# Optimization experiments

Measured on AMD Instinct MI355X. Metric: run time of the kernel, lower is better.

Reference implementation:

```python
import jax, jax.numpy as jnp
import numpy as np

N_NODES = 50000
N_EDGES = 800000
N_GRAPHS = 256


def setup_inputs() -> dict:
    key = jax.random.key(0)
    ks = jax.random.split(key, 20)
    s = 0.05
    return {
        "x": jax.random.normal(ks[0], (N_NODES, 128), jnp.float32),
        "edge_index": jax.random.randint(ks[1], (2, N_EDGES), 0, N_NODES, jnp.int64),
        "batch_index": jnp.sort(jax.random.randint(ks[2], (N_NODES,), 0, N_GRAPHS, jnp.int64)),
        "mol_features": jax.random.normal(ks[3], (N_GRAPHS, 256), jnp.float32),
        "gcn_W": jax.random.normal(ks[4], (3, 128, 128), jnp.float32) * s,
        "gcn_b": jax.random.normal(ks[5], (3, 128), jnp.float32) * s,
        "gcn_out_W": jax.random.normal(ks[6], (128, 128), jnp.float32) * s,
        "gcn_out_b": jax.random.normal(ks[7], (128,), jnp.float32) * s,
        "mlp_W": jax.random.normal(ks[8], (2, 256, 256), jnp.float32) * s,
        "mlp_b": jax.random.normal(ks[9], (2, 256), jnp.float32) * s,
        "mlp_out_W": jax.random.normal(ks[10], (64, 256), jnp.float32) * s,
        "mlp_out_b": jax.random.normal(ks[11], (64,), jnp.float32) * s,
        "pred_W1": jax.random.normal(ks[12], (256, 192), jnp.float32) * s,
        "pred_b1": jax.random.normal(ks[13], (256,), jnp.float32) * s,
        "pred_W2": jax.random.normal(ks[14], (256, 256), jnp.float32) * s,
        "pred_b2": jax.random.normal(ks[15], (256,), jnp.float32) * s,
        "out_W": jax.random.normal(ks[16], (1, 256), jnp.float32) * s,
        "out_b": jax.random.normal(ks[17], (1,), jnp.float32) * s,
    }


def reference(x, edge_index, batch_index, mol_features,
              gcn_W, gcn_b, gcn_out_W, gcn_out_b,
              mlp_W, mlp_b, mlp_out_W, mlp_out_b,
              pred_W1, pred_b1, pred_W2, pred_b2, out_W, out_b):
    N = x.shape[0]
    E = edge_index.shape[1]
    G = mol_features.shape[0]
    row, col = edge_index[0], edge_index[1]

    # GCN normalization with self-loops (PyG gcn_norm, symmetric):
    # deg[i] = in-degree(i) + 1 (self loop); norm_e = d^-1/2[row] * d^-1/2[col]
    deg = jax.ops.segment_sum(jnp.ones((E,), x.dtype), col, num_segments=N) + 1.0
    dinv = jax.lax.rsqrt(deg)
    enorm = (dinv[row] * dinv[col])[:, None]     # [E,1]
    self_c = (dinv * dinv)[:, None]              # [N,1] self-loop coefficient

    h1 = x
    for i in range(gcn_W.shape[0]):
        h = h1 @ gcn_W[i].T                      # per-node transform [N,128]
        agg = jax.ops.segment_sum(h[row] * enorm, col, num_segments=N)
        h1 = jax.nn.relu(agg + self_c * h + gcn_b[i])
    h1 = h1 @ gcn_out_W.T + gcn_out_b            # final GCN-branch Linear (no relu)

    # global_mean_pool over batch_index -> [G,128]
    sums = jax.ops.segment_sum(h1, batch_index, num_segments=G)
    counts = jax.ops.segment_sum(jnp.ones((N,), x.dtype), batch_index, num_segments=G)
    h1 = sums / jnp.maximum(counts, 1.0)[:, None]

    # MLP branch: relu after every linear (including last)
    h2 = mol_features
    for i in range(mlp_W.shape[0]):
        h2 = jax.nn.relu(h2 @ mlp_W[i].T + mlp_b[i])
    h2 = jax.nn.relu(h2 @ mlp_out_W.T + mlp_out_b)

    h = jnp.concatenate([h1, h2], axis=1)        # [G,192]
    h = jax.nn.relu(h @ pred_W1.T + pred_b1)
    h = jax.nn.relu(h @ pred_W2.T + pred_b2)
    return h @ out_W.T + out_b                   # [G,1]
```

## Files before the change

### kernel.cpp

```cpp
#include <hip/hip_runtime.h>


typedef __attribute__((ext_vector_type(8))) short short8;
typedef __attribute__((ext_vector_type(4))) float f32x4;

__device__ __forceinline__ unsigned short f2bf(float f) {
    union { float f; unsigned u; } c; c.f = f;
    unsigned u = c.u;
    unsigned r = u + 0x7FFFu + ((u >> 16) & 1u);
    return (unsigned short)(r >> 16);
}
__device__ __forceinline__ float bflo(unsigned w) {
    union { unsigned u; float f; } c; c.u = w << 16; return c.f;
}
__device__ __forceinline__ float bfhi(unsigned w) {
    union { unsigned u; float f; } c; c.u = w & 0xFFFF0000u; return c.f;
}

__global__ void k_zero(int* deg, float* pool, float* cnt, int* csr_pad,
                       int N, int G) {
    int i = blockIdx.x * blockDim.x + threadIdx.x;
    if (i < N) deg[i] = 0;
    if (i < G * 128) pool[i] = 0.f;
    if (i < G) cnt[i] = 0.f;
    if (i < 32) csr_pad[i] = 0;
}

__global__ void k_castx(const float* __restrict__ x, unsigned short* __restrict__ xb,
                        int total8) {
    int i = blockIdx.x * blockDim.x + threadIdx.x;
    if (i >= total8) return;
    const float4* s = (const float4*)(x + (size_t)i * 8);
    float4 a = s[0], b = s[1];
    uint4 o;
    o.x = ((unsigned)f2bf(a.y) << 16) | f2bf(a.x);
    o.y = ((unsigned)f2bf(a.w) << 16) | f2bf(a.z);
    o.z = ((unsigned)f2bf(b.y) << 16) | f2bf(b.x);
    o.w = ((unsigned)f2bf(b.w) << 16) | f2bf(b.z);
    *(uint4*)(xb + (size_t)i * 8) = o;
}

__global__ void k_wcast(const float* __restrict__ gcnW, uint4* __restrict__ Wb) {
    int cid = blockIdx.x * 256 + threadIdx.x;
    if (cid >= 3 * 2048) return;
    int l = cid >> 11, rem = cid & 2047;
    int o = rem >> 4, c = rem & 15;
    const float4* s = (const float4*)(gcnW + (size_t)l * 16384 + o * 128 + c * 8);
    float4 a = s[0], b = s[1];
    uint4 v;
    v.x = ((unsigned)f2bf(a.y) << 16) | f2bf(a.x);
    v.y = ((unsigned)f2bf(a.w) << 16) | f2bf(a.z);
    v.z = ((unsigned)f2bf(b.y) << 16) | f2bf(b.x);
    v.w = ((unsigned)f2bf(b.w) << 16) | f2bf(b.z);
    Wb[(l << 11) | (o << 4) | (c ^ (o & 15))] = v;
}

__global__ void k_degree(const int* __restrict__ col, int* __restrict__ deg, int E) {
    int e = blockIdx.x * blockDim.x + threadIdx.x;
    if (e < E) atomicAdd(&deg[col[e]], 1);
}

__global__ __launch_bounds__(256) void k_scan1(const int* __restrict__ deg,
                                               int* __restrict__ bsum, int N) {
    int t = threadIdx.x;
    int i = blockIdx.x * 256 + t;
    int v = (i < N) ? deg[i] : 0;
    #pragma unroll
    for (int off = 32; off > 0; off >>= 1) v += __shfl_xor(v, off, 64);
    __shared__ int ws[4];
    if ((t & 63) == 0) ws[t >> 6] = v;
    __syncthreads();
    if (t == 0) bsum[blockIdx.x] = ws[0] + ws[1] + ws[2] + ws[3];
}

__global__ __launch_bounds__(256) void k_scan2(int* __restrict__ bsum, int NB) {
    int t = threadIdx.x, lane = t & 63, wv = t >> 6;
    int v = (t < NB) ? bsum[t] : 0;
    int x = v;
    #pragma unroll
    for (int off = 1; off < 64; off <<= 1) {
        int u = __shfl_up(x, off, 64);
        if (lane >= off) x += u;
    }
    __shared__ int ws[4];
    if (lane == 63) ws[wv] = x;
    __syncthreads();
    int woff = 0;
    for (int w = 0; w < wv; ++w) woff += ws[w];
    if (t < NB) bsum[t] = woff + x - v;
}

__global__ __launch_bounds__(256) void k_scan3(const int* __restrict__ deg,
                                               const int* __restrict__ bsum,
                                               int* __restrict__ rowptr,
                                               int* __restrict__ cursor,
                                               float* __restrict__ dinv,
                                               int N, int E) {
    int t = threadIdx.x, lane = t & 63, wv = t >> 6;
    int i = blockIdx.x * 256 + t;
    int v = (i < N) ? deg[i] : 0;
    int x = v;
    #pragma unroll
    for (int off = 1; off < 64; off <<= 1) {
        int u = __shfl_up(x, off, 64);
        if (lane >= off) x += u;
    }
    __shared__ int ws[4];
    if (lane == 63) ws[wv] = x;
    __syncthreads();
    int woff = 0;
    for (int w = 0; w < wv; ++w) woff += ws[w];
    int excl = bsum[blockIdx.x] + woff + (x - v);
    if (i < N) {
        rowptr[i] = excl;
        cursor[i] = excl;
        dinv[i] = rsqrtf((float)v + 1.0f);
    }
    if (i == 0) rowptr[N] = E;
}

__global__ void k_scatter(const int* __restrict__ row, const int* __restrict__ col,
                          const float* __restrict__ dinv,
                          int* __restrict__ cursor,
                          unsigned long long* __restrict__ csr, int E) {
    int e = blockIdx.x * blockDim.x + threadIdx.x;
    if (e < E) {
        int pos = atomicAdd(&cursor[col[e]], 1);
        int r = row[e];
        union { float f; unsigned u; } w; w.f = dinv[r];
        csr[pos] = ((unsigned long long)(unsigned)r << 32) | w.u;
    }
}

__global__ __launch_bounds__(256) void k_agg(const unsigned short* __restrict__ h,
                                             unsigned short* __restrict__ y,
                                             const float* __restrict__ dinv,
                                             const int* __restrict__ rowptr,
                                             const uint2* __restrict__ csr,
                                             int N) {
    const int lane = threadIdx.x & 63;
    const int n = blockIdx.x * 4 + (threadIdx.x >> 6);
    if (n >= N) return;
    const int fg = lane & 15;
    const int slot = lane >> 4;
    const int s = rowptr[n], e = rowptr[n + 1];

    float acc[8] = {0.f, 0.f, 0.f, 0.f, 0.f, 0.f, 0.f, 0.f};
    for (int base = s; base < e; base += 16) {
        int li = base + fg;
        uint2 pk = csr[li];
        float w_l = (li < e) ? bflo(pk.x >> 16) : 0.f;
        w_l = (li < e) ? __uint_as_float(pk.x) : 0.f;
        int src_l = (int)pk.y;
        #pragma unroll
        for (int i = 0; i < 4; ++i) {
            int j = i * 4 + slot;
            int src = __shfl(src_l, j, 16);
            float w = __shfl(w_l, j, 16);
            uint4 v = *(const uint4*)(h + (size_t)src * 128 + fg * 8);
            acc[0] += w * bflo(v.x); acc[1] += w * bfhi(v.x);
            acc[2] += w * bflo(v.y); acc[3] += w * bfhi(v.y);
            acc[4] += w * bflo(v.z); acc[5] += w * bfhi(v.z);
            acc[6] += w * bflo(v.w); acc[7] += w * bfhi(v.w);
        }
    }
    #pragma unroll
    for (int r = 0; r < 8; ++r) {
        acc[r] += __shfl_xor(acc[r], 16, 64);
        acc[r] += __shfl_xor(acc[r], 32, 64);
    }
    if (slot == 0) {
        float dn = dinv[n], dn2 = dn * dn;
        uint4 hv = *(const uint4*)(h + (size_t)n * 128 + fg * 8);
        float sv[8] = {bflo(hv.x), bfhi(hv.x), bflo(hv.y), bfhi(hv.y),
                       bflo(hv.z), bfhi(hv.z), bflo(hv.w), bfhi(hv.w)};
        unsigned short ob[8];
        #pragma unroll
        for (int r = 0; r < 8; ++r) ob[r] = f2bf(acc[r] * dn + dn2 * sv[r]);
        uint4 o;
        o.x = ((unsigned)ob[1] << 16) | ob[0];
        o.y = ((unsigned)ob[3] << 16) | ob[2];
        o.z = ((unsigned)ob[5] << 16) | ob[4];
        o.w = ((unsigned)ob[7] << 16) | ob[6];
        *(uint4*)(y + (size_t)n * 128 + fg * 8) = o;
    }
}

__global__ __launch_bounds__(256) void k_mm(const unsigned short* __restrict__ A,
                                            const uint4* __restrict__ Wb,
                                            const float* __restrict__ bias,
                                            unsigned short* __restrict__ C, int N) {
    __shared__ uint4 Wsh[2048];
    const int tid = threadIdx.x;
    #pragma unroll
    for (int it = 0; it < 8; ++it)
        Wsh[tid + it * 256] = Wb[tid + it * 256];

    const int lane = tid & 63;
    const int wv = tid >> 6;
    const int l15 = lane & 15, quad = lane >> 4;
    const int arow_i = blockIdx.x * 64 + wv * 16 + l15;
    const unsigned short* arow = A + (size_t)min(arow_i, N - 1) * 128;

    f32x4 acc[8];
    #pragma unroll
    for (int ct = 0; ct < 8; ++ct) acc[ct] = (f32x4){0.f, 0.f, 0.f, 0.f};

    __syncthreads();
    #pragma unroll
    for (int kiter = 0; kiter < 4; ++kiter) {
        short8 af = *(const short8*)(arow + kiter * 32 + quad * 8);
        const int cswz = (kiter * 4 + quad) ^ l15;
        #pragma unroll
        for (int ct = 0; ct < 8; ++ct) {
            short8 bf = *(const short8*)(&Wsh[((ct * 16 + l15) << 4) | cswz]);
            acc[ct] = __builtin_amdgcn_mfma_f32_16x16x32_bf16(af, bf, acc[ct], 0, 0, 0);
        }
    }

    const int rbase = blockIdx.x * 64 + wv * 16 + quad * 4;
    #pragma unroll
    for (int ct = 0; ct < 8; ++ct) {
        int colc = ct * 16 + l15;
        float bcol = bias[colc];
        #pragma unroll
        for (int r = 0; r < 4; ++r) {
            int rr = rbase + r;
            if (rr < N) {
                float v = fmaxf(acc[ct][r] + bcol, 0.f);
                C[(size_t)rr * 128 + colc] = f2bf(v);
            }
        }
    }
}

__global__ __launch_bounds__(256) void k_pool(const unsigned short* __restrict__ h,
                                              const int* __restrict__ batch,
                                              float* __restrict__ pool,
                                              float* __restrict__ cnt, int N) {
    int t = threadIdx.x;
    int fg = t & 15, sg = t >> 4;
    int n0 = blockIdx.x * 512 + sg * 32;
    if (n0 >= N) return;
    int n1 = min(n0 + 32, N);
    int gprev = batch[n0];
    float racc[8] = {0.f, 0.f, 0.f, 0.f, 0.f, 0.f, 0.f, 0.f};
    float rcnt = 0.f;
    for (int n = n0; n < n1; ++n) {
        int g = batch[n];
        if (g != gprev) {
            float* dst = pool + (size_t)gprev * 128 + fg * 8;
            #pragma unroll
            for (int r = 0; r < 8; ++r) atomicAdd(dst + r, racc[r]);
            if (fg == 0) atomicAdd(&cnt[gprev], rcnt);
            #pragma unroll
            for (int r = 0; r < 8; ++r) racc[r] = 0.f;
            rcnt = 0.f; gprev = g;
        }
        uint4 v = *(const uint4*)(h + (size_t)n * 128 + fg * 8);
        racc[0] += bflo(v.x); racc[1] += bfhi(v.x);
        racc[2] += bflo(v.y); racc[3] += bfhi(v.y);
        racc[4] += bflo(v.z); racc[5] += bfhi(v.z);
        racc[6] += bflo(v.w); racc[7] += bfhi(v.w);
        rcnt += 1.f;
    }
    float* dst = pool + (size_t)gprev * 128 + fg * 8;
    #pragma unroll
    for (int r = 0; r < 8; ++r) atomicAdd(dst + r, racc[r]);
    if (fg == 0) atomicAdd(&cnt[gprev], rcnt);
}

__global__ __launch_bounds__(256) void k_head(
    const float* __restrict__ pool, const float* __restrict__ cnt,
    const float* __restrict__ gcnoW, const float* __restrict__ gcnob,
    const float* __restrict__ mol,
    const float* __restrict__ mlpW, const float* __restrict__ mlpb,
    const float* __restrict__ mloW, const float* __restrict__ mlob,
    const float* __restrict__ pW1, const float* __restrict__ pb1,
    const float* __restrict__ pW2, const float* __restrict__ pb2,
    const float* __restrict__ oW, const float* __restrict__ ob,
    float* __restrict__ out) {
    int g = blockIdx.x, t = threadIdx.x;
    __shared__ float s0[256], s1[256], s2[192], mean[128], red[256];

    s0[t] = mol[(size_t)g * 256 + t];
    if (t < 128) {
        float c = cnt[g];
        mean[t] = pool[(size_t)g * 128 + t] / fmaxf(c, 1.f);
    }
    __syncthreads();

    float acc = mlpb[t];
    {
        const float4* w = (const float4*)(mlpW + (size_t)t * 256);
        #pragma unroll 4
        for (int k4 = 0; k4 < 64; ++k4) {
            float4 wv = w[k4];
            acc += s0[k4*4+0]*wv.x + s0[k4*4+1]*wv.y + s0[k4*4+2]*wv.z + s0[k4*4+3]*wv.w;
        }
    }
    s1[t] = fmaxf(acc, 0.f);
    __syncthreads();

    acc = mlpb[256 + t];
    {
        const float4* w = (const float4*)(mlpW + 65536 + (size_t)t * 256);
        #pragma unroll 4
        for (int k4 = 0; k4 < 64; ++k4) {
            float4 wv = w[k4];
            acc += s1[k4*4+0]*wv.x + s1[k4*4+1]*wv.y + s1[k4*4+2]*wv.z + s1[k4*4+3]*wv.w;
        }
    }
    s0[t] = fmaxf(acc, 0.f);
    __syncthreads();

    if (t < 64) {
        float a2 = mlob[t];
        const float4* w = (const float4*)(mloW + (size_t)t * 256);
        #pragma unroll 4
        for (int k4 = 0; k4 < 64; ++k4) {
            float4 wv = w[k4];
            a2 += s0[k4*4+0]*wv.x + s0[k4*4+1]*wv.y + s0[k4*4+2]*wv.z + s0[k4*4+3]*wv.w;
        }
        s2[128 + t] = fmaxf(a2, 0.f);
    } else if (t < 192) {
        int o = t - 64;
        float a2 = gcnob[o];
        const float4* w = (const float4*)(gcnoW + (size_t)o * 128);
        #pragma unroll 4
        for (int k4 = 0; k4 < 32; ++k4) {
            float4 wv = w[k4];
            a2 += mean[k4*4+0]*wv.x + mean[k4*4+1]*wv.y + mean[k4*4+2]*wv.z + mean[k4*4+3]*wv.w;
        }
        s2[o] = a2;
    }
    __syncthreads();

    acc = pb1[t];
    {
        const float4* w = (const float4*)(pW1 + (size_t)t * 192);
        #pragma unroll 4
        for (int k4 = 0; k4 < 48; ++k4) {
            float4 wv = w[k4];
            acc += s2[k4*4+0]*wv.x + s2[k4*4+1]*wv.y + s2[k4*4+2]*wv.z + s2[k4*4+3]*wv.w;
        }
    }
    s1[t] = fmaxf(acc, 0.f);
    __syncthreads();

    acc = pb2[t];
    {
        const float4* w = (const float4*)(pW2 + (size_t)t * 256);
        #pragma unroll 4
        for (int k4 = 0; k4 < 64; ++k4) {
            float4 wv = w[k4];
            acc += s1[k4*4+0]*wv.x + s1[k4*4+1]*wv.y + s1[k4*4+2]*wv.z + s1[k4*4+3]*wv.w;
        }
    }
    s0[t] = fmaxf(acc, 0.f);
    __syncthreads();

    red[t] = s0[t] * oW[t];
    __syncthreads();
    for (int off = 128; off > 0; off >>= 1) {
        if (t < off) red[t] += red[t + off];
        __syncthreads();
    }
    if (t == 0) out[g] = red[0] + ob[0];
}

extern "C" void kernel_launch(void* const* d_in, const int* in_sizes, int n_in,
                              void* d_out, int out_size, void* d_ws, size_t ws_size,
                              hipStream_t stream) {
    const float* x     = (const float*)d_in[0];
    const int*   ei    = (const int*)d_in[1];
    const int*   batch = (const int*)d_in[2];
    const float* mol   = (const float*)d_in[3];
    const float* gcnW  = (const float*)d_in[4];
    const float* gcnb  = (const float*)d_in[5];
    const float* gcnoW = (const float*)d_in[6];
    const float* gcnob = (const float*)d_in[7];
    const float* mlpW  = (const float*)d_in[8];
    const float* mlpb  = (const float*)d_in[9];
    const float* mloW  = (const float*)d_in[10];
    const float* mlob  = (const float*)d_in[11];
    const float* pW1   = (const float*)d_in[12];
    const float* pb1   = (const float*)d_in[13];
    const float* pW2   = (const float*)d_in[14];
    const float* pb2   = (const float*)d_in[15];
    const float* oW    = (const float*)d_in[16];
    const float* ob    = (const float*)d_in[17];

    const int N = in_sizes[0] / 128;
    const int E = in_sizes[1] / 2;
    const int G = in_sizes[3] / 256;
    const int* row = ei;
    const int* col = ei + E;

    char* p = (char*)d_ws;
    auto alloc = [&](size_t bytes) {
        char* q = p;
        p += (bytes + 255) & ~(size_t)255;
        return (void*)q;
    };
    int*    deg    = (int*)alloc((size_t)N * 4);
    int*    rowptr = (int*)alloc((size_t)(N + 1) * 4);
    int*    cursor = (int*)alloc((size_t)N * 4);
    unsigned long long* csr = (unsigned long long*)alloc((size_t)(E + 16) * 8);
    float*  dinv   = (float*)alloc((size_t)N * 4);
    unsigned short* xb   = (unsigned short*)alloc((size_t)N * 128 * 2);
    unsigned short* bufA = (unsigned short*)alloc((size_t)N * 128 * 2);
    unsigned short* bufB = (unsigned short*)alloc((size_t)N * 128 * 2);
    uint4*  Wb     = (uint4*)alloc((size_t)3 * 2048 * 16);
    float*  pool   = (float*)alloc((size_t)G * 128 * 4);
    float*  cnt    = (float*)alloc((size_t)G * 4);
    int*    bsum   = (int*)alloc(256 * 4);

    const int NB = (N + 255) / 256;

    k_zero<<<NB, 256, 0, stream>>>(deg, pool, cnt, (int*)(csr + E), N, G);
    k_castx<<<(N * 16 + 255) / 256, 256, 0, stream>>>(x, xb, N * 16);
    k_wcast<<<24, 256, 0, stream>>>(gcnW, Wb);
    k_degree<<<(E + 255) / 256, 256, 0, stream>>>(col, deg, E);
    k_scan1<<<NB, 256, 0, stream>>>(deg, bsum, N);
    k_scan2<<<1, 256, 0, stream>>>(bsum, NB);
    k_scan3<<<NB, 256, 0, stream>>>(deg, bsum, rowptr, cursor, dinv, N, E);
    k_scatter<<<(E + 255) / 256, 256, 0, stream>>>(row, col, dinv, cursor, csr, E);

    const int mmblocks = (N + 63) / 64;
    const int aggblocks = (N + 3) / 4;
    const unsigned short* src = xb;
    for (int l = 0; l < 3; ++l) {
        k_agg<<<aggblocks, 256, 0, stream>>>(src, bufA, dinv, rowptr,
                                             (const uint2*)csr, N);
        k_mm<<<mmblocks, 256, 0, stream>>>(bufA, Wb + (size_t)l * 2048,
                                           gcnb + (size_t)l * 128, bufB, N);
        src = bufB;
    }
    k_pool<<<(N + 511) / 512, 256, 0, stream>>>(bufB, batch, pool, cnt, N);
    k_head<<<G, 256, 0, stream>>>(pool, cnt, gcnoW, gcnob, mol, mlpW, mlpb,
                                  mloW, mlob, pW1, pb1, pW2, pb2, oW, ob,
                                  (float*)d_out);
}
```

Measured before the change: 394.1 us.

## Build CSR via bucketed counting sort, use 16-bit indices, fold dinv into features

Replaces the per-node atomic degree/scan/scatter CSR build with a bucketed two-level counting sort. Edges are histogrammed and binned per 64-node bucket, then sorted locally in shared memory. Neighbour lists shrink to 16-bit source indices with no per-edge weight. The symmetric normalisation is folded into the features instead: x is pre-scaled by dinv, each GEMM epilogue multiplies by dinv, and aggregation scales by dinv[n] once. This cuts edge-list bandwidth and per-edge multiplies. In exchange it assumes N < 65536 and that the bucket count fits a fixed 784-entry shared histogram, and it adds a single-block scan.

```diff
diff --git a/kernel.cpp b/kernel.cpp
--- a/kernel.cpp
+++ b/kernel.cpp
@@ -3,6 +3,10 @@
 
 typedef __attribute__((ext_vector_type(8))) short short8;
 typedef __attribute__((ext_vector_type(4))) float f32x4;
+
+#define BKT 64
+#define SL 8
+#define NBINBLK 256
 
 __device__ __forceinline__ unsigned short f2bf(float f) {
     union { float f; unsigned u; } c; c.f = f;
@@ -17,26 +21,128 @@
     union { unsigned u; float f; } c; c.u = w & 0xFFFF0000u; return c.f;
 }
 
-__global__ void k_zero(int* deg, float* pool, float* cnt, int* csr_pad,
-                       int N, int G) {
+__global__ void k_zero(int* ghist, float* pool, float* cnt, int* csr_pad,
+                       int M, int N, int G) {
     int i = blockIdx.x * blockDim.x + threadIdx.x;
-    if (i < N) deg[i] = 0;
+    if (i < M) ghist[i] = 0;
     if (i < G * 128) pool[i] = 0.f;
     if (i < G) cnt[i] = 0.f;
-    if (i < 32) csr_pad[i] = 0;
-}
-
-__global__ void k_castx(const float* __restrict__ x, unsigned short* __restrict__ xb,
-                        int total8) {
+    if (i < 8) csr_pad[i] = 0;
+}
+
+__global__ __launch_bounds__(256) void k_hist(const int* __restrict__ col,
+                                              int* __restrict__ ghist,
+                                              int E, int C, int NBK) {
+    __shared__ int h[784];
+    int t = threadIdx.x;
+    for (int i = t; i < NBK; i += 256) h[i] = 0;
+    __syncthreads();
+    const int x = blockIdx.x & (SL - 1);
+    int e0 = blockIdx.x * C, e1 = min(E, e0 + C);
+    for (int e = e0 + t; e < e1; e += 256) atomicAdd(&h[col[e] >> 6], 1);
+    __syncthreads();
+    for (int b = t; b < NBK; b += 256) {
+        int c = h[b];
+        if (c) atomicAdd(&ghist[b * SL + x], c);
+    }
+}
+
+__global__ __launch_bounds__(256) void k_bscan(const int* __restrict__ ghist,
+                                               int* __restrict__ gbase,
+                                               int* __restrict__ cur,
+                                               int* __restrict__ rowptr,
+                                               int M, int N, int E) {
+    __shared__ int ws[4];
+    __shared__ int s_carry;
+    int t = threadIdx.x, lane = t & 63, wv = t >> 6;
+    if (t == 0) s_carry = 0;
+    __syncthreads();
+    for (int base = 0; base < M; base += 256) {
+        int i = base + t;
+        int v = (i < M) ? ghist[i] : 0;
+        int x = v;
+        #pragma unroll
+        for (int off = 1; off < 64; off <<= 1) {
+            int u = __shfl_up(x, off, 64);
+            if (lane >= off) x += u;
+        }
+        if (lane == 63) ws[wv] = x;
+        __syncthreads();
+        int woff = 0;
+        for (int w = 0; w < wv; ++w) woff += ws[w];
+        int excl = s_carry + woff + (x - v);
+        if (i < M) { gbase[i] = excl; cur[i] = excl; }
+        __syncthreads();
+        if (t == 255) s_carry = excl + v;
+        __syncthreads();
+    }
+    if (t == 0) { gbase[M] = E; rowptr[N] = E; }
+}
+
+__global__ __launch_bounds__(256) void k_bin(const int* __restrict__ row,
+                                             const int* __restrict__ col,
+                                             int* __restrict__ cur,
+                                             unsigned* __restrict__ gbin,
+                                             int E, int C) {
+    const int x = blockIdx.x & (SL - 1);
+    int e0 = blockIdx.x * C, e1 = min(E, e0 + C);
+    for (int e = e0 + threadIdx.x; e < e1; e += 256) {
+        int c = col[e];
+        int si = (c >> 6) * SL + x;
+        int pos = atomicAdd(&cur[si], 1);
+        gbin[pos] = (unsigned)row[e] | ((unsigned)(c & 63) << 16);
+    }
+}
+
+__global__ __launch_bounds__(256) void k_csr(const unsigned* __restrict__ gbin,
+                                             const int* __restrict__ gbase,
+                                             int* __restrict__ rowptr,
+                                             float* __restrict__ dinv,
+                                             unsigned short* __restrict__ csrf,
+                                             int N) {
+    const int b = blockIdx.x, t = threadIdx.x;
+    __shared__ int cnt[64], lcur[64];
+    if (t < 64) cnt[t] = 0;
+    __syncthreads();
+    const int beg = gbase[b * SL], end = gbase[(b + 1) * SL];
+    for (int i = beg + t; i < end; i += 256)
+        atomicAdd(&cnt[gbin[i] >> 16], 1);
+    __syncthreads();
+    if (t < 64) {
+        int v = cnt[t], x = v;
+        #pragma unroll
+        for (int off = 1; off < 64; off <<= 1) {
+            int u = __shfl_up(x, off, 64);
+            if (t >= off) x += u;
+        }
+        int excl = x - v;
+        lcur[t] = excl;
+        int node = b * 64 + t;
+        if (node < N) {
+            rowptr[node] = beg + excl;
+            dinv[node] = rsqrtf((float)v + 1.0f);
+        }
+    }
+    __syncthreads();
+    for (int i = beg + t; i < end; i += 256) {
+        unsigned v = gbin[i];
+        int p = atomicAdd(&lcur[v >> 16], 1);
+        csrf[beg + p] = (unsigned short)(v & 0xFFFFu);
+    }
+}
+
+__global__ void k_castx(const float* __restrict__ x, const float* __restrict__ dinv,
+                        unsigned short* __restrict__ xb, int total8) {
     int i = blockIdx.x * blockDim.x + threadIdx.x;
     if (i >= total8) return;
+    float d = dinv[i >> 4];
     const float4* s = (const float4*)(x + (size_t)i * 8);
     float4 a = s[0], b = s[1];
     uint4 o;
-    o.x = ((unsigned)f2bf(a.y) << 16) | f2bf(a.x);
-    o.y = ((unsigned)f2bf(a.w) << 16) | f2bf(a.z);
-    o.z = ((unsigned)f2bf(b.y) << 16) | f2bf(b.x);
-    o.w = ((unsigned)f2bf(b.w) << 16) | f2bf(b.z);
+    o.x = ((unsigned)f2bf(d * a.y) << 16) | f2bf(d * a.x);
+    o.y = ((unsigned)f2bf(d * a.w) << 16) | f2bf(d * a.z);
+    o.z = ((unsigned)f2bf(d * b.y) << 16) | f2bf(d * b.x);
+    o.w = ((unsigned)f2bf(d * b.w) << 16) | f2bf(d * b.z);
     *(uint4*)(xb + (size_t)i * 8) = o;
 }
 
@@ -55,88 +161,11 @@
     Wb[(l << 11) | (o << 4) | (c ^ (o & 15))] = v;
 }
 
-__global__ void k_degree(const int* __restrict__ col, int* __restrict__ deg, int E) {
-    int e = blockIdx.x * blockDim.x + threadIdx.x;
-    if (e < E) atomicAdd(&deg[col[e]], 1);
-}
-
-__global__ __launch_bounds__(256) void k_scan1(const int* __restrict__ deg,
-                                               int* __restrict__ bsum, int N) {
-    int t = threadIdx.x;
-    int i = blockIdx.x * 256 + t;
-    int v = (i < N) ? deg[i] : 0;
-    #pragma unroll
-    for (int off = 32; off > 0; off >>= 1) v += __shfl_xor(v, off, 64);
-    __shared__ int ws[4];
-    if ((t & 63) == 0) ws[t >> 6] = v;
-    __syncthreads();
-    if (t == 0) bsum[blockIdx.x] = ws[0] + ws[1] + ws[2] + ws[3];
-}
-
-__global__ __launch_bounds__(256) void k_scan2(int* __restrict__ bsum, int NB) {
-    int t = threadIdx.x, lane = t & 63, wv = t >> 6;
-    int v = (t < NB) ? bsum[t] : 0;
-    int x = v;
-    #pragma unroll
-    for (int off = 1; off < 64; off <<= 1) {
-        int u = __shfl_up(x, off, 64);
-        if (lane >= off) x += u;
-    }
-    __shared__ int ws[4];
-    if (lane == 63) ws[wv] = x;
-    __syncthreads();
-    int woff = 0;
-    for (int w = 0; w < wv; ++w) woff += ws[w];
-    if (t < NB) bsum[t] = woff + x - v;
-}
-
-__global__ __launch_bounds__(256) void k_scan3(const int* __restrict__ deg,
-                                               const int* __restrict__ bsum,
-                                               int* __restrict__ rowptr,
-                                               int* __restrict__ cursor,
-                                               float* __restrict__ dinv,
-                                               int N, int E) {
-    int t = threadIdx.x, lane = t & 63, wv = t >> 6;
-    int i = blockIdx.x * 256 + t;
-    int v = (i < N) ? deg[i] : 0;
-    int x = v;
-    #pragma unroll
-    for (int off = 1; off < 64; off <<= 1) {
-        int u = __shfl_up(x, off, 64);
-        if (lane >= off) x += u;
-    }
-    __shared__ int ws[4];
-    if (lane == 63) ws[wv] = x;
-    __syncthreads();
-    int woff = 0;
-    for (int w = 0; w < wv; ++w) woff += ws[w];
-    int excl = bsum[blockIdx.x] + woff + (x - v);
-    if (i < N) {
-        rowptr[i] = excl;
-        cursor[i] = excl;
-        dinv[i] = rsqrtf((float)v + 1.0f);
-    }
-    if (i == 0) rowptr[N] = E;
-}
-
-__global__ void k_scatter(const int* __restrict__ row, const int* __restrict__ col,
-                          const float* __restrict__ dinv,
-                          int* __restrict__ cursor,
-                          unsigned long long* __restrict__ csr, int E) {
-    int e = blockIdx.x * blockDim.x + threadIdx.x;
-    if (e < E) {
-        int pos = atomicAdd(&cursor[col[e]], 1);
-        int r = row[e];
-        union { float f; unsigned u; } w; w.f = dinv[r];
-        csr[pos] = ((unsigned long long)(unsigned)r << 32) | w.u;
-    }
-}
-
 __global__ __launch_bounds__(256) void k_agg(const unsigned short* __restrict__ h,
                                              unsigned short* __restrict__ y,
                                              const float* __restrict__ dinv,
                                              const int* __restrict__ rowptr,
-                                             const uint2* __restrict__ csr,
+                                             const unsigned short* __restrict__ csrf,
                                              int N) {
     const int lane = threadIdx.x & 63;
     const int n = blockIdx.x * 4 + (threadIdx.x >> 6);
@@ -147,21 +176,19 @@
 
     float acc[8] = {0.f, 0.f, 0.f, 0.f, 0.f, 0.f, 0.f, 0.f};
     for (int base = s; base < e; base += 16) {
-        int li = base + fg;
-        uint2 pk = csr[li];
-        float w_l = (li < e) ? bflo(pk.x >> 16) : 0.f;
-        w_l = (li < e) ? __uint_as_float(pk.x) : 0.f;
-        int src_l = (int)pk.y;
+        int src_l = csrf[base + fg];
         #pragma unroll
         for (int i = 0; i < 4; ++i) {
             int j = i * 4 + slot;
             int src = __shfl(src_l, j, 16);
-            float w = __shfl(w_l, j, 16);
             uint4 v = *(const uint4*)(h + (size_t)src * 128 + fg * 8);
-            acc[0] += w * bflo(v.x); acc[1] += w * bfhi(v.x);
-            acc[2] += w * bflo(v.y); acc[3] += w * bfhi(v.y);
-            acc[4] += w * bflo(v.z); acc[5] += w * bfhi(v.z);
-            acc[6] += w * bflo(v.w); acc[7] += w * bfhi(v.w);
+            bool ok = (base + j) < e;
+            v.x = ok ? v.x : 0u; v.y = ok ? v.y : 0u;
+            v.z = ok ? v.z : 0u; v.w = ok ? v.w : 0u;
+            acc[0] += bflo(v.x); acc[1] += bfhi(v.x);
+            acc[2] += bflo(v.y); acc[3] += bfhi(v.y);
+            acc[4] += bflo(v.z); acc[5] += bfhi(v.z);
+            acc[6] += bflo(v.w); acc[7] += bfhi(v.w);
         }
     }
     #pragma unroll
@@ -170,13 +197,13 @@
         acc[r] += __shfl_xor(acc[r], 32, 64);
     }
     if (slot == 0) {
-        float dn = dinv[n], dn2 = dn * dn;
+        float dn = dinv[n];
         uint4 hv = *(const uint4*)(h + (size_t)n * 128 + fg * 8);
         float sv[8] = {bflo(hv.x), bfhi(hv.x), bflo(hv.y), bfhi(hv.y),
                        bflo(hv.z), bfhi(hv.z), bflo(hv.w), bfhi(hv.w)};
         unsigned short ob[8];
         #pragma unroll
-        for (int r = 0; r < 8; ++r) ob[r] = f2bf(acc[r] * dn + dn2 * sv[r]);
+        for (int r = 0; r < 8; ++r) ob[r] = f2bf(dn * (acc[r] + sv[r]));
         uint4 o;
         o.x = ((unsigned)ob[1] << 16) | ob[0];
         o.y = ((unsigned)ob[3] << 16) | ob[2];
@@ -189,6 +216,7 @@
 __global__ __launch_bounds__(256) void k_mm(const unsigned short* __restrict__ A,
                                             const uint4* __restrict__ Wb,
                                             const float* __restrict__ bias,
+                                            const float* __restrict__ dscale,
                                             unsigned short* __restrict__ C, int N) {
     __shared__ uint4 Wsh[2048];
     const int tid = threadIdx.x;
@@ -219,6 +247,12 @@
     }
 
     const int rbase = blockIdx.x * 64 + wv * 16 + quad * 4;
+    float ds[4];
+    #pragma unroll
+    for (int r = 0; r < 4; ++r) {
+        int rr = rbase + r;
+        ds[r] = (dscale && rr < N) ? dscale[rr] : 1.f;
+    }
     #pragma unroll
     for (int ct = 0; ct < 8; ++ct) {
         int colc = ct * 16 + l15;
@@ -227,7 +261,7 @@
         for (int r = 0; r < 4; ++r) {
             int rr = rbase + r;
             if (rr < N) {
-                float v = fmaxf(acc[ct][r] + bcol, 0.f);
+                float v = fmaxf(acc[ct][r] + bcol, 0.f) * ds[r];
                 C[(size_t)rr * 128 + colc] = f2bf(v);
             }
         }
@@ -397,44 +431,49 @@
     const int* row = ei;
     const int* col = ei + E;
 
+    const int NBK = (N + BKT - 1) / BKT;
+    const int M = NBK * SL;
+    const int C = (E + NBINBLK - 1) / NBINBLK;
+
     char* p = (char*)d_ws;
     auto alloc = [&](size_t bytes) {
         char* q = p;
         p += (bytes + 255) & ~(size_t)255;
         return (void*)q;
     };
-    int*    deg    = (int*)alloc((size_t)N * 4);
     int*    rowptr = (int*)alloc((size_t)(N + 1) * 4);
-    int*    cursor = (int*)alloc((size_t)N * 4);
-    unsigned long long* csr = (unsigned long long*)alloc((size_t)(E + 16) * 8);
     float*  dinv   = (float*)alloc((size_t)N * 4);
+    int*    ghist  = (int*)alloc((size_t)M * 4);
+    int*    gbase  = (int*)alloc((size_t)(M + 1) * 4);
+    int*    cur    = (int*)alloc((size_t)M * 4);
+    unsigned* gbin = (unsigned*)alloc((size_t)E * 4);
+    unsigned short* csrf = (unsigned short*)alloc((size_t)(E + 16) * 2);
     unsigned short* xb   = (unsigned short*)alloc((size_t)N * 128 * 2);
     unsigned short* bufA = (unsigned short*)alloc((size_t)N * 128 * 2);
     unsigned short* bufB = (unsigned short*)alloc((size_t)N * 128 * 2);
     uint4*  Wb     = (uint4*)alloc((size_t)3 * 2048 * 16);
     float*  pool   = (float*)alloc((size_t)G * 128 * 4);
     float*  cnt    = (float*)alloc((size_t)G * 4);
-    int*    bsum   = (int*)alloc(256 * 4);
 
     const int NB = (N + 255) / 256;
 
-    k_zero<<<NB, 256, 0, stream>>>(deg, pool, cnt, (int*)(csr + E), N, G);
-    k_castx<<<(N * 16 + 255) / 256, 256, 0, stream>>>(x, xb, N * 16);
+    k_zero<<<NB, 256, 0, stream>>>(ghist, pool, cnt, (int*)(csrf + E), M, N, G);
     k_wcast<<<24, 256, 0, stream>>>(gcnW, Wb);
-    k_degree<<<(E + 255) / 256, 256, 0, stream>>>(col, deg, E);
-    k_scan1<<<NB, 256, 0, stream>>>(deg, bsum, N);
-    k_scan2<<<1, 256, 0, stream>>>(bsum, NB);
-    k_scan3<<<NB, 256, 0, stream>>>(deg, bsum, rowptr, cursor, dinv, N, E);
-    k_scatter<<<(E + 255) / 256, 256, 0, stream>>>(row, col, dinv, cursor, csr, E);
+    k_hist<<<NBINBLK, 256, 0, stream>>>(col, ghist, E, C, NBK);
+    k_bscan<<<1, 256, 0, stream>>>(ghist, gbase, cur, rowptr, M, N, E);
+    k_bin<<<NBINBLK, 256, 0, stream>>>(row, col, cur, gbin, E, C);
+    k_csr<<<NBK, 256, 0, stream>>>(gbin, gbase, rowptr, dinv, csrf, N);
+    k_castx<<<(N * 16 + 255) / 256, 256, 0, stream>>>(x, dinv, xb, N * 16);
 
     const int mmblocks = (N + 63) / 64;
     const int aggblocks = (N + 3) / 4;
     const unsigned short* src = xb;
     for (int l = 0; l < 3; ++l) {
-        k_agg<<<aggblocks, 256, 0, stream>>>(src, bufA, dinv, rowptr,
-                                             (const uint2*)csr, N);
+        k_agg<<<aggblocks, 256, 0, stream>>>(src, bufA, dinv, rowptr, csrf, N);
         k_mm<<<mmblocks, 256, 0, stream>>>(bufA, Wb + (size_t)l * 2048,
-                                           gcnb + (size_t)l * 128, bufB, N);
+                                           gcnb + (size_t)l * 128,
+                                           (l < 2) ? dinv : (const float*)nullptr,
+                                           bufB, N);
         src = bufB;
     }
     k_pool<<<(N + 511) / 512, 256, 0, stream>>>(bufB, batch, pool, cnt, N);
```

New measurement: 397.8 us. About the same (+0.9%).
